# Kernel tuning notes

Hardware: AMD Instinct MI355X
Metric: run time of the kernel (lower is better)

The kernel has to match this reference:

```python
import jax, jax.numpy as jnp
import numpy as np

B, N, H, NH = 8, 1024, 512, 8
DK = H // NH


def setup_inputs() -> dict:
    key = jax.random.key(0)
    ks = jax.random.split(key, 6)
    x = jax.random.normal(ks[0], (B, N, H), dtype=jnp.float32)
    adj = jax.random.randint(ks[1], (B, N, N), 0, 2, dtype=jnp.int32)
    # ensure no all-zero row (self-loops) so softmax is well-defined
    adj = jnp.maximum(adj, jnp.eye(N, dtype=jnp.int32)[None])
    s = 1.0 / np.sqrt(H)
    Wq = jax.random.normal(ks[2], (H, H), dtype=jnp.float32) * s
    Wk = jax.random.normal(ks[3], (H, H), dtype=jnp.float32) * s
    Wv = jax.random.normal(ks[4], (H, H), dtype=jnp.float32) * s
    Wg = jax.random.normal(ks[5], (H, 2 * H), dtype=jnp.float32) * (1.0 / np.sqrt(2 * H))
    bg = jnp.zeros((H,), dtype=jnp.float32)
    return {"x": x, "adj": adj, "Wq": Wq, "Wk": Wk, "Wv": Wv, "Wg": Wg, "bg": bg}


def reference(x, adj, Wq, Wk, Wv, Wg, bg):
    b, n, h = x.shape
    # projections (nn.Linear: x @ W.T), split heads -> [b, n, nh, dk]
    q = (x @ Wq.T).reshape(b, n, NH, DK)
    k = (x @ Wk.T).reshape(b, n, NH, DK)
    v = (x @ Wv.T).reshape(b, n, NH, DK)
    # scaled masked attention: [b, nh, n, n]
    scores = jnp.einsum('bqhd,bkhd->bhqk', q, k) / jnp.sqrt(jnp.float32(DK))
    mask = (adj != 0)[:, None, :, :]
    scores = jnp.where(mask, scores, -jnp.inf)
    attn = jax.nn.softmax(scores, axis=-1)  # dropout p=0.0 -> identity
    c = jnp.einsum('bhqk,bkhd->bqhd', attn, v).reshape(b, n, h)
    # sigmoid gated residual combine
    gate = jax.nn.sigmoid(jnp.concatenate([c, x], axis=2) @ Wg.T + bg)
    return gate * x + (1.0 - gate) * c
```

## Files before the change

kernel.cpp:

```cpp
#include <hip/hip_runtime.h>
#include <math.h>

#define B_  8
#define N_  1024
#define H_  512
#define NH_ 8
#define DK_ 64
#define M_  (B_ * N_)

typedef __attribute__((ext_vector_type(4))) float f32x4;
typedef __attribute__((ext_vector_type(8))) short bf16x8;

__device__ __forceinline__ unsigned short f2bf(float f) {
    unsigned int u = __float_as_uint(f);
    u = (u + 0x7fffu + ((u >> 16) & 1u)) >> 16;
    return (unsigned short)u;
}

__device__ __forceinline__ float bf2f(unsigned short s) {
    return __uint_as_float(((unsigned int)s) << 16);
}

__device__ __forceinline__ float fexp2(float x) {
#if __has_builtin(__builtin_amdgcn_exp2f)
    return __builtin_amdgcn_exp2f(x);
#else
    return exp2f(x);
#endif
}

__device__ __forceinline__ void gload16(const unsigned short* g, unsigned short* l) {
    __builtin_amdgcn_global_load_lds(
        (const __attribute__((address_space(1))) void*)g,
        (__attribute__((address_space(3))) void*)l, 16, 0, 0);
}

__global__ __launch_bounds__(256) void prep_k(const float* __restrict__ x,
                                              const float* __restrict__ Wq,
                                              const float* __restrict__ Wk,
                                              const float* __restrict__ Wv,
                                              const float* __restrict__ Wg,
                                              const int*   __restrict__ adj,
                                              unsigned short* __restrict__ xb,
                                              unsigned short* __restrict__ wqb,
                                              unsigned short* __restrict__ wkb,
                                              unsigned short* __restrict__ wvb,
                                              unsigned short* __restrict__ wgb,
                                              unsigned long long* __restrict__ mb)
{
    int id = blockIdx.x;
    if (id >= 5376) {
        int gw   = (id - 5376) * 4 + (threadIdx.x >> 6);
        int lane = threadIdx.x & 63;
        int kt = gw & 15;
        int q  = (gw >> 4) & (N_ - 1);
        int b  = gw >> 14;
        int val = adj[(size_t)(b * N_ + q) * N_ + kt * 64 + lane];
        unsigned long long m = __ballot(val != 0);
        if (lane == 0) mb[gw] = m;
        return;
    }
    const float* src; unsigned short* dst; int off; float scale = 1.0f;
    if (id < 4096)      { src = x;  dst = xb;  off = id; }
    else if (id < 4352) { src = Wq; dst = wqb; off = id - 4096; scale = 0.18033688011112042f; }
    else if (id < 4608) { src = Wk; dst = wkb; off = id - 4352; }
    else if (id < 4864) { src = Wv; dst = wvb; off = id - 4608; }
    else                { src = Wg; dst = wgb; off = id - 4864; }
    size_t i = (size_t)off * 1024 + threadIdx.x * 4;
    float4 v = *(const float4*)&src[i];
    *(ushort4*)&dst[i] = make_ushort4(f2bf(v.x * scale), f2bf(v.y * scale),
                                      f2bf(v.z * scale), f2bf(v.w * scale));
}

__global__ __launch_bounds__(256, 3) void proj_k(const unsigned short* __restrict__ xb,
                                                 const unsigned short* __restrict__ Wqb,
                                                 const unsigned short* __restrict__ Wkb,
                                                 const unsigned short* __restrict__ Wvb,
                                                 unsigned short* __restrict__ qk,
                                                 unsigned short* __restrict__ vt)
{
    __shared__ unsigned short As[2][4096];
    __shared__ unsigned short Bs[2][4096];
    const int tid = threadIdx.x;
    const int lane = tid & 63, wv = tid >> 6;
    const int ln = lane & 15, quad = lane >> 4;
    const int wm = wv >> 1, wn = wv & 1;
    const int row0 = blockIdx.x * 128;
    const int w    = blockIdx.y >> 2;
    const int col0 = (blockIdx.y & 3) * 128;
    const unsigned short* W = (w == 0) ? Wqb : ((w == 1) ? Wkb : Wvb);
    f32x4 acc[4][4] = {};

    auto issue = [&](int t, int bi) {
        int kt = t * 32;
        #pragma unroll
        for (int i = 0; i < 2; ++i) {
            int c = tid + i * 256;
            int c4 = c >> 7, row = c & 127;
            gload16(&xb[(size_t)(row0 + row) * H_ + kt + c4 * 8], &As[bi][c * 8]);
            gload16(&W [(size_t)(col0 + row) * H_ + kt + c4 * 8], &Bs[bi][c * 8]);
        }
    };

    issue(0, 0);
    for (int t = 0; t < 16; ++t) {
        __syncthreads();
        if (t < 15) issue(t + 1, (t + 1) & 1);
        const unsigned short* Ac = As[t & 1];
        const unsigned short* Bc = Bs[t & 1];
        bf16x8 af[4], bf[4];
        #pragma unroll
        for (int u = 0; u < 4; ++u) {
            af[u] = *(const bf16x8*)&Ac[(quad * 128 + wm * 64 + u * 16 + ln) * 8];
            bf[u] = *(const bf16x8*)&Bc[(quad * 128 + wn * 64 + u * 16 + ln) * 8];
        }
        #pragma unroll
        for (int mt = 0; mt < 4; ++mt)
            #pragma unroll
            for (int nt = 0; nt < 4; ++nt)
                acc[mt][nt] = __builtin_amdgcn_mfma_f32_16x16x32_bf16(af[mt], bf[nt], acc[mt][nt], 0, 0, 0);
    }

    if (w < 2) {
        #pragma unroll
        for (int mt = 0; mt < 4; ++mt)
            #pragma unroll
            for (int nt = 0; nt < 4; ++nt)
                #pragma unroll
                for (int r = 0; r < 4; ++r) {
                    int m = row0 + wm * 64 + mt * 16 + quad * 4 + r;
                    int c = w * H_ + col0 + wn * 64 + nt * 16 + ln;
                    qk[(size_t)m * (2 * H_) + c] = f2bf(acc[mt][nt][r]);
                }
    } else {
        #pragma unroll
        for (int mt = 0; mt < 4; ++mt)
            #pragma unroll
            for (int nt = 0; nt < 4; ++nt) {
                int c = col0 + wn * 64 + nt * 16 + ln;
                int head = c >> 6, d = c & 63;
                int m0 = row0 + wm * 64 + mt * 16 + quad * 4;
                int bb = m0 >> 10, n = m0 & (N_ - 1);
                ushort4 u = make_ushort4(f2bf(acc[mt][nt][0]), f2bf(acc[mt][nt][1]),
                                         f2bf(acc[mt][nt][2]), f2bf(acc[mt][nt][3]));
                *(ushort4*)&vt[((size_t)(bb * NH_ + head) * DK_ + d) * N_ + n] = u;
            }
    }
}

__global__ __launch_bounds__(256, 3) void attn_k(const unsigned short* __restrict__ qk,
                                                 const unsigned short* __restrict__ Vt,
                                                 const unsigned long long* __restrict__ Mb,
                                                 unsigned short* __restrict__ Cmb)
{
    const int qt   = blockIdx.x & 15;
    const int head = (blockIdx.x >> 4) & 7;
    const int b    = blockIdx.x >> 7;

    __shared__ unsigned short Ks[2][4096];
    __shared__ unsigned short Vs[2][4096];
    __shared__ unsigned short Ps[4][16][72];

    const int tid = threadIdx.x;
    const int lane = tid & 63, wv = tid >> 6;
    const int ln = lane & 15, quad = lane >> 4;
    const int q = qt * 64 + wv * 16 + ln;

    const unsigned short* Qrow = &qk[(size_t)(b * N_ + q) * (2 * H_) + head * DK_];
    bf16x8 bq[2];
    bq[0] = *(const bf16x8*)&Qrow[quad * 8];
    bq[1] = *(const bf16x8*)&Qrow[32 + quad * 8];

    const unsigned short* Kb = &qk[(size_t)(b * N_) * (2 * H_) + H_ + head * DK_];
    const unsigned short* Vb = &Vt[(size_t)(b * NH_ + head) * DK_ * N_];
    const unsigned long long* mrow = &Mb[(size_t)(b * N_ + q) * 16];

    f32x4 o[4] = {};
    float psum = 0.f;

    auto issue = [&](int t, int bi) {
        #pragma unroll
        for (int i = 0; i < 2; ++i) {
            int c = tid + i * 256;
            int c8 = c >> 6, row = c & 63;
            gload16(&Kb[(size_t)(t * 64 + row) * (2 * H_) + c8 * 8], &Ks[bi][c * 8]);
            gload16(&Vb[(size_t)row * N_ + t * 64 + c8 * 8], &Vs[bi][c * 8]);
        }
    };

    issue(0, 0);

    for (int t = 0; t < 16; ++t) {
        __syncthreads();
        if (t < 15) issue(t + 1, (t + 1) & 1);
        const unsigned short* Kc = Ks[t & 1];
        const unsigned short* Vc = Vs[t & 1];
        unsigned long long mq = mrow[t];

        f32x4 s[4] = {};
        #pragma unroll
        for (int kk = 0; kk < 2; ++kk)
            #pragma unroll
            for (int nt = 0; nt < 4; ++nt) {
                bf16x8 ka = *(const bf16x8*)&Kc[((kk * 4 + quad) * 64 + nt * 16 + ln) * 8];
                s[nt] = __builtin_amdgcn_mfma_f32_16x16x32_bf16(ka, bq[kk], s[nt], 0, 0, 0);
            }

        unsigned long long sh = mq >> (quad * 4);
        #pragma unroll
        for (int nt = 0; nt < 4; ++nt) {
            unsigned int bn = (unsigned int)(sh >> (nt * 16)) & 0xFu;
            float p[4];
            #pragma unroll
            for (int r = 0; r < 4; ++r) {
                float e = fexp2(s[nt][r]);
                p[r] = (bn & (1u << r)) ? e : 0.f;
                psum += p[r];
            }
            unsigned int d0 = __builtin_amdgcn_perm(__float_as_uint(p[1]), __float_as_uint(p[0]), 0x07060302u);
            unsigned int d1 = __builtin_amdgcn_perm(__float_as_uint(p[3]), __float_as_uint(p[2]), 0x07060302u);
            *(uint2*)&Ps[wv][ln][nt * 16 + quad * 4] = make_uint2(d0, d1);
        }

        bf16x8 pb[2];
        pb[0] = *(const bf16x8*)&Ps[wv][ln][quad * 8];
        pb[1] = *(const bf16x8*)&Ps[wv][ln][32 + quad * 8];

        #pragma unroll
        for (int kk = 0; kk < 2; ++kk)
            #pragma unroll
            for (int dt = 0; dt < 4; ++dt) {
                bf16x8 va = *(const bf16x8*)&Vc[((kk * 4 + quad) * 64 + dt * 16 + ln) * 8];
                o[dt] = __builtin_amdgcn_mfma_f32_16x16x32_bf16(va, pb[kk], o[dt], 0, 0, 0);
            }
    }

    psum += __shfl_xor(psum, 16);
    psum += __shfl_xor(psum, 32);
    float inv = 1.f / psum;

    #pragma unroll
    for (int dt = 0; dt < 4; ++dt) {
        ushort4 u = make_ushort4(f2bf(o[dt][0] * inv), f2bf(o[dt][1] * inv),
                                 f2bf(o[dt][2] * inv), f2bf(o[dt][3] * inv));
        *(ushort4*)&Cmb[(size_t)(b * N_ + q) * H_ + head * DK_ + dt * 16 + quad * 4] = u;
    }
}

__global__ __launch_bounds__(256, 3) void gate_k(const unsigned short* __restrict__ cmb,
                                                 const unsigned short* __restrict__ xb,
                                                 const unsigned short* __restrict__ Wgb,
                                                 const float* __restrict__ bgp,
                                                 float* __restrict__ out)
{
    __shared__ unsigned short As[2][4096];
    __shared__ unsigned short Bs[2][2048];
    const int tid = threadIdx.x;
    const int lane = tid & 63, wv = tid >> 6;
    const int ln = lane & 15, quad = lane >> 4;
    const int wm = wv >> 1, wn = wv & 1;
    const int row0 = blockIdx.x * 128;
    const int col0 = blockIdx.y * 64;
    f32x4 acc[4][2] = {};

    auto issue = [&](int t, int bi) {
        const unsigned short* Asrc = (t < 16) ? cmb : xb;
        int ko = (t * 32) & (H_ - 1);
        #pragma unroll
        for (int i = 0; i < 2; ++i) {
            int c = tid + i * 256;
            int c4 = c >> 7, row = c & 127;
            gload16(&Asrc[(size_t)(row0 + row) * H_ + ko + c4 * 8], &As[bi][c * 8]);
        }
        {
            int c = tid & 255;
            int c4 = c >> 6, row = c & 63;
            if (tid < 256)
                gload16(&Wgb[(size_t)(col0 + row) * (2 * H_) + t * 32 + c4 * 8], &Bs[bi][c * 8]);
        }
    };

    issue(0, 0);
    for (int t = 0; t < 32; ++t) {
        __syncthreads();
        if (t < 31) issue(t + 1, (t + 1) & 1);
        const unsigned short* Ac = As[t & 1];
        const unsigned short* Bc = Bs[t & 1];
        bf16x8 af[4], bf[2];
        #pragma unroll
        for (int u = 0; u < 4; ++u)
            af[u] = *(const bf16x8*)&Ac[(quad * 128 + wm * 64 + u * 16 + ln) * 8];
        #pragma unroll
        for (int u = 0; u < 2; ++u)
            bf[u] = *(const bf16x8*)&Bc[(quad * 64 + wn * 32 + u * 16 + ln) * 8];
        #pragma unroll
        for (int mt = 0; mt < 4; ++mt)
            #pragma unroll
            for (int nt = 0; nt < 2; ++nt)
                acc[mt][nt] = __builtin_amdgcn_mfma_f32_16x16x32_bf16(af[mt], bf[nt], acc[mt][nt], 0, 0, 0);
    }

    #pragma unroll
    for (int mt = 0; mt < 4; ++mt)
        #pragma unroll
        for (int nt = 0; nt < 2; ++nt)
            #pragma unroll
            for (int r = 0; r < 4; ++r) {
                int m = row0 + wm * 64 + mt * 16 + quad * 4 + r;
                int c = col0 + wn * 32 + nt * 16 + ln;
                float g  = 1.f / (1.f + __expf(-(acc[mt][nt][r] + bgp[c])));
                float xv = bf2f(xb[(size_t)m * H_ + c]);
                float cv = bf2f(cmb[(size_t)m * H_ + c]);
                out[(size_t)m * H_ + c] = g * xv + (1.f - g) * cv;
            }
}

extern "C" void kernel_launch(void* const* d_in, const int* in_sizes, int n_in,
                              void* d_out, int out_size, void* d_ws, size_t ws_size,
                              hipStream_t stream)
{
    const float* x   = (const float*)d_in[0];
    const int*   adj = (const int*)  d_in[1];
    const float* Wq  = (const float*)d_in[2];
    const float* Wk  = (const float*)d_in[3];
    const float* Wv  = (const float*)d_in[4];
    const float* Wg  = (const float*)d_in[5];
    const float* bg  = (const float*)d_in[6];
    float* out = (float*)d_out;

    unsigned short* xb  = (unsigned short*)d_ws;
    unsigned short* wqb = xb  + (size_t)M_ * H_;
    unsigned short* wkb = wqb + (size_t)H_ * H_;
    unsigned short* wvb = wkb + (size_t)H_ * H_;
    unsigned short* wgb = wvb + (size_t)H_ * H_;
    unsigned short* qk  = wgb + (size_t)H_ * 2 * H_;
    unsigned short* vt  = qk  + (size_t)M_ * 2 * H_;
    unsigned short* cmb = vt  + (size_t)M_ * H_;
    unsigned long long* mb = (unsigned long long*)(cmb + (size_t)M_ * H_);

    prep_k<<<5376 + 32768, 256, 0, stream>>>(x, Wq, Wk, Wv, Wg, adj,
                                             xb, wqb, wkb, wvb, wgb, mb);

    proj_k<<<dim3(M_ / 128, 12), 256, 0, stream>>>(xb, wqb, wkb, wvb, qk, vt);

    attn_k<<<B_ * NH_ * (N_ / 64), 256, 0, stream>>>(qk, vt, mb, cmb);

    gate_k<<<dim3(M_ / 128, H_ / 64), 256, 0, stream>>>(cmb, xb, wgb, bg, out);
}
```

Measured before the change: 230.4 us.

## Process 128 queries per attention block and batch adjacency mask rows per block

The attention kernel now handles two 16-query groups per wave (128 queries per block), so each K/V tile staged in shared memory is reused across twice as many queries, halving K/V global traffic and block count. The block index order is changed so consecutive blocks cover different batch-head pairs for the same query tile. The mask-building part of prep_k now processes a full adjacency row per block with four ballots per wave, cutting the grid size. This doubles per-thread accumulator registers and leaves half as many attention blocks, which may reduce occupancy and load balance.

```diff
diff --git a/kernel.cpp b/kernel.cpp
--- a/kernel.cpp
+++ b/kernel.cpp
@@ -50,14 +50,17 @@
 {
     int id = blockIdx.x;
     if (id >= 5376) {
-        int gw   = (id - 5376) * 4 + (threadIdx.x >> 6);
+        int row  = id - 5376;
+        int wv   = threadIdx.x >> 6;
         int lane = threadIdx.x & 63;
-        int kt = gw & 15;
-        int q  = (gw >> 4) & (N_ - 1);
-        int b  = gw >> 14;
-        int val = adj[(size_t)(b * N_ + q) * N_ + kt * 64 + lane];
-        unsigned long long m = __ballot(val != 0);
-        if (lane == 0) mb[gw] = m;
+        const int* arow = &adj[(size_t)row * N_];
+        #pragma unroll
+        for (int j = 0; j < 4; ++j) {
+            int kt = wv * 4 + j;
+            int val = arow[kt * 64 + lane];
+            unsigned long long m = __ballot(val != 0);
+            if (lane == 0) mb[(size_t)row * 16 + kt] = m;
+        }
         return;
     }
     const float* src; unsigned short* dst; int off; float scale = 1.0f;
@@ -153,38 +156,41 @@
                                                  const unsigned long long* __restrict__ Mb,
                                                  unsigned short* __restrict__ Cmb)
 {
-    const int qt   = blockIdx.x & 15;
-    const int head = (blockIdx.x >> 4) & 7;
-    const int b    = blockIdx.x >> 7;
+    const int bh   = blockIdx.x & 63;
+    const int qt   = blockIdx.x >> 6;
+    const int b    = bh >> 3;
+    const int head = bh & 7;
 
     __shared__ unsigned short Ks[2][4096];
     __shared__ unsigned short Vs[2][4096];
-    __shared__ unsigned short Ps[4][16][72];
+    __shared__ unsigned short Ps[4][2][16][72];
 
     const int tid = threadIdx.x;
     const int lane = tid & 63, wv = tid >> 6;
     const int ln = lane & 15, quad = lane >> 4;
-    const int q = qt * 64 + wv * 16 + ln;
-
-    const unsigned short* Qrow = &qk[(size_t)(b * N_ + q) * (2 * H_) + head * DK_];
-    bf16x8 bq[2];
-    bq[0] = *(const bf16x8*)&Qrow[quad * 8];
-    bq[1] = *(const bf16x8*)&Qrow[32 + quad * 8];
-
-    const unsigned short* Kb = &qk[(size_t)(b * N_) * (2 * H_) + H_ + head * DK_];
-    const unsigned short* Vb = &Vt[(size_t)(b * NH_ + head) * DK_ * N_];
-    const unsigned long long* mrow = &Mb[(size_t)(b * N_ + q) * 16];
-
-    f32x4 o[4] = {};
-    float psum = 0.f;
+    const int q0 = qt * 128 + wv * 32 + ln;
+    const int q1 = q0 + 16;
+
+    const unsigned short* Kbase = qk + H_ + head * DK_;
+    const unsigned short* Vbase = Vt + (size_t)(b * NH_ + head) * DK_ * N_;
+
+    bf16x8 bq[2][2];
+    #pragma unroll
+    for (int kk = 0; kk < 2; ++kk) {
+        bq[0][kk] = *(const bf16x8*)&qk[(size_t)(b * N_ + q0) * (2 * H_) + head * DK_ + kk * 32 + quad * 8];
+        bq[1][kk] = *(const bf16x8*)&qk[(size_t)(b * N_ + q1) * (2 * H_) + head * DK_ + kk * 32 + quad * 8];
+    }
+
+    f32x4 o[2][4] = {};
+    float psum[2] = {0.f, 0.f};
 
     auto issue = [&](int t, int bi) {
         #pragma unroll
         for (int i = 0; i < 2; ++i) {
             int c = tid + i * 256;
             int c8 = c >> 6, row = c & 63;
-            gload16(&Kb[(size_t)(t * 64 + row) * (2 * H_) + c8 * 8], &Ks[bi][c * 8]);
-            gload16(&Vb[(size_t)row * N_ + t * 64 + c8 * 8], &Vs[bi][c * 8]);
+            gload16(&Kbase[(size_t)(b * N_ + t * 64 + row) * (2 * H_) + c8 * 8], &Ks[bi][c * 8]);
+            gload16(&Vbase[(size_t)row * N_ + t * 64 + c8 * 8], &Vs[bi][c * 8]);
         }
     };
 
@@ -195,55 +201,69 @@
         if (t < 15) issue(t + 1, (t + 1) & 1);
         const unsigned short* Kc = Ks[t & 1];
         const unsigned short* Vc = Vs[t & 1];
-        unsigned long long mq = mrow[t];
-
-        f32x4 s[4] = {};
+
+        unsigned long long mq[2];
+        mq[0] = Mb[(size_t)(b * N_ + q0) * 16 + t];
+        mq[1] = Mb[(size_t)(b * N_ + q1) * 16 + t];
+
+        f32x4 s[2][4] = {};
         #pragma unroll
         for (int kk = 0; kk < 2; ++kk)
             #pragma unroll
             for (int nt = 0; nt < 4; ++nt) {
                 bf16x8 ka = *(const bf16x8*)&Kc[((kk * 4 + quad) * 64 + nt * 16 + ln) * 8];
-                s[nt] = __builtin_amdgcn_mfma_f32_16x16x32_bf16(ka, bq[kk], s[nt], 0, 0, 0);
-            }
-
-        unsigned long long sh = mq >> (quad * 4);
-        #pragma unroll
-        for (int nt = 0; nt < 4; ++nt) {
-            unsigned int bn = (unsigned int)(sh >> (nt * 16)) & 0xFu;
-            float p[4];
-            #pragma unroll
-            for (int r = 0; r < 4; ++r) {
-                float e = fexp2(s[nt][r]);
-                p[r] = (bn & (1u << r)) ? e : 0.f;
-                psum += p[r];
-            }
-            unsigned int d0 = __builtin_amdgcn_perm(__float_as_uint(p[1]), __float_as_uint(p[0]), 0x07060302u);
-            unsigned int d1 = __builtin_amdgcn_perm(__float_as_uint(p[3]), __float_as_uint(p[2]), 0x07060302u);
-            *(uint2*)&Ps[wv][ln][nt * 16 + quad * 4] = make_uint2(d0, d1);
-        }
-
-        bf16x8 pb[2];
-        pb[0] = *(const bf16x8*)&Ps[wv][ln][quad * 8];
-        pb[1] = *(const bf16x8*)&Ps[wv][ln][32 + quad * 8];
+                s[0][nt] = __builtin_amdgcn_mfma_f32_16x16x32_bf16(ka, bq[0][kk], s[0][nt], 0, 0, 0);
+                s[1][nt] = __builtin_amdgcn_mfma_f32_16x16x32_bf16(ka, bq[1][kk], s[1][nt], 0, 0, 0);
+            }
+
+        #pragma unroll
+        for (int g = 0; g < 2; ++g) {
+            unsigned long long sh = mq[g] >> (quad * 4);
+            #pragma unroll
+            for (int nt = 0; nt < 4; ++nt) {
+                unsigned int bn = (unsigned int)(sh >> (nt * 16)) & 0xFu;
+                float p[4];
+                #pragma unroll
+                for (int r = 0; r < 4; ++r) {
+                    float e = fexp2(s[g][nt][r]);
+                    p[r] = (bn & (1u << r)) ? e : 0.f;
+                    psum[g] += p[r];
+                }
+                unsigned int d0 = __builtin_amdgcn_perm(__float_as_uint(p[1]), __float_as_uint(p[0]), 0x07060302u);
+                unsigned int d1 = __builtin_amdgcn_perm(__float_as_uint(p[3]), __float_as_uint(p[2]), 0x07060302u);
+                *(uint2*)&Ps[wv][g][ln][nt * 16 + quad * 4] = make_uint2(d0, d1);
+            }
+        }
+
+        bf16x8 pb[2][2];
+        #pragma unroll
+        for (int g = 0; g < 2; ++g)
+            #pragma unroll
+            for (int kk = 0; kk < 2; ++kk)
+                pb[g][kk] = *(const bf16x8*)&Ps[wv][g][ln][kk * 32 + quad * 8];
 
         #pragma unroll
         for (int kk = 0; kk < 2; ++kk)
             #pragma unroll
             for (int dt = 0; dt < 4; ++dt) {
                 bf16x8 va = *(const bf16x8*)&Vc[((kk * 4 + quad) * 64 + dt * 16 + ln) * 8];
-                o[dt] = __builtin_amdgcn_mfma_f32_16x16x32_bf16(va, pb[kk], o[dt], 0, 0, 0);
-            }
-    }
-
-    psum += __shfl_xor(psum, 16);
-    psum += __shfl_xor(psum, 32);
-    float inv = 1.f / psum;
+                o[0][dt] = __builtin_amdgcn_mfma_f32_16x16x32_bf16(va, pb[0][kk], o[0][dt], 0, 0, 0);
+                o[1][dt] = __builtin_amdgcn_mfma_f32_16x16x32_bf16(va, pb[1][kk], o[1][dt], 0, 0, 0);
+            }
+    }
 
     #pragma unroll
-    for (int dt = 0; dt < 4; ++dt) {
-        ushort4 u = make_ushort4(f2bf(o[dt][0] * inv), f2bf(o[dt][1] * inv),
-                                 f2bf(o[dt][2] * inv), f2bf(o[dt][3] * inv));
-        *(ushort4*)&Cmb[(size_t)(b * N_ + q) * H_ + head * DK_ + dt * 16 + quad * 4] = u;
+    for (int g = 0; g < 2; ++g) {
+        psum[g] += __shfl_xor(psum[g], 16);
+        psum[g] += __shfl_xor(psum[g], 32);
+        float inv = 1.f / psum[g];
+        int qg = (g == 0) ? q0 : q1;
+        #pragma unroll
+        for (int dt = 0; dt < 4; ++dt) {
+            ushort4 u = make_ushort4(f2bf(o[g][dt][0] * inv), f2bf(o[g][dt][1] * inv),
+                                     f2bf(o[g][dt][2] * inv), f2bf(o[g][dt][3] * inv));
+            *(ushort4*)&Cmb[(size_t)(b * N_ + qg) * H_ + head * DK_ + dt * 16 + quad * 4] = u;
+        }
     }
 }
 
@@ -338,12 +358,12 @@
     unsigned short* cmb = vt  + (size_t)M_ * H_;
     unsigned long long* mb = (unsigned long long*)(cmb + (size_t)M_ * H_);
 
-    prep_k<<<5376 + 32768, 256, 0, stream>>>(x, Wq, Wk, Wv, Wg, adj,
-                                             xb, wqb, wkb, wvb, wgb, mb);
+    prep_k<<<5376 + 8192, 256, 0, stream>>>(x, Wq, Wk, Wv, Wg, adj,
+                                            xb, wqb, wkb, wvb, wgb, mb);
 
     proj_k<<<dim3(M_ / 128, 12), 256, 0, stream>>>(xb, wqb, wkb, wvb, qk, vt);
 
-    attn_k<<<B_ * NH_ * (N_ / 64), 256, 0, stream>>>(qk, vt, mb, cmb);
+    attn_k<<<B_ * NH_ * (N_ / 128), 256, 0, stream>>>(qk, vt, mb, cmb);
 
     gate_k<<<dim3(M_ / 128, H_ / 64), 256, 0, stream>>>(cmb, xb, wgb, bg, out);
 }
```

Result: faster. 201.3 us (-12.6%).
